# Performance work log

Hardware: AMD Instinct MI355X
Metric: run time of the kernel (lower is better)

## Reference

```python
import jax, jax.numpy as jnp
import numpy as np

N, E, G = 50000, 640000, 256
NODE_IN, EDGE_IN, EXT_IN = 32, 16, 8
H, L = 128, 3
BN_EPS = 1e-5


def _linear_init(key, fan_in, fan_out):
    kw, kb = jax.random.split(key)
    s = 1.0 / np.sqrt(fan_in)
    w = jax.random.uniform(kw, (fan_in, fan_out), minval=-s, maxval=s, dtype=jnp.float32)
    b = jax.random.uniform(kb, (fan_out,), minval=-s, maxval=s, dtype=jnp.float32)
    return w, b


def setup_inputs() -> dict:
    key = jax.random.key(0)
    ks = jax.random.split(key, 16)
    x = jax.random.normal(ks[0], (N, NODE_IN), dtype=jnp.float32)
    edge_index = jax.random.randint(ks[1], (2, E), 0, N)
    edge_attr = jax.random.normal(ks[2], (E, EDGE_IN), dtype=jnp.float32)
    batch = jnp.sort(jax.random.randint(ks[3], (N,), 0, G))
    externals = jax.random.normal(ks[4], (G, EXT_IN), dtype=jnp.float32)

    node_w, node_b = _linear_init(ks[5], NODE_IN, H)
    ee_w1, ee_b1 = _linear_init(ks[6], EDGE_IN, H)
    ee_w2, ee_b2 = _linear_init(ks[7], H, H)
    # stacked per-layer GINEConv MLP params: [L, H, H] / [L, H]
    cks = jax.random.split(ks[8], 2 * L)
    cw1, cb1, cw2, cb2 = [], [], [], []
    for l in range(L):
        w1, b1 = _linear_init(cks[2 * l], H, H)
        w2, b2 = _linear_init(cks[2 * l + 1], H, H)
        cw1.append(w1); cb1.append(b1); cw2.append(w2); cb2.append(b2)
    conv_w1 = jnp.stack(cw1); conv_b1 = jnp.stack(cb1)
    conv_w2 = jnp.stack(cw2); conv_b2 = jnp.stack(cb2)
    bn_gamma = jnp.ones((L, H), dtype=jnp.float32)
    bn_beta = jnp.zeros((L, H), dtype=jnp.float32)
    ext_w1, ext_b1 = _linear_init(ks[9], EXT_IN, H)
    ext_w2, ext_b2 = _linear_init(ks[10], H, H)
    reg_w1, reg_b1 = _linear_init(ks[11], 2 * H, H)
    reg_w2, reg_b2 = _linear_init(ks[12], H, 1)

    return dict(x=x, edge_attr=edge_attr, externals=externals,
                node_w=node_w, node_b=node_b,
                ee_w1=ee_w1, ee_b1=ee_b1, ee_w2=ee_w2, ee_b2=ee_b2,
                conv_w1=conv_w1, conv_b1=conv_b1, conv_w2=conv_w2, conv_b2=conv_b2,
                bn_gamma=bn_gamma, bn_beta=bn_beta,
                ext_w1=ext_w1, ext_b1=ext_b1, ext_w2=ext_w2, ext_b2=ext_b2,
                reg_w1=reg_w1, reg_b1=reg_b1, reg_w2=reg_w2, reg_b2=reg_b2,
                edge_index=edge_index, batch=batch, num_graphs=G)


def reference(x, edge_attr, externals,
              node_w, node_b, ee_w1, ee_b1, ee_w2, ee_b2,
              conv_w1, conv_b1, conv_w2, conv_b2, bn_gamma, bn_beta,
              ext_w1, ext_b1, ext_w2, ext_b2,
              reg_w1, reg_b1, reg_w2, reg_b2,
              edge_index, batch, num_graphs):
    n = x.shape[0]
    src, dst = edge_index[0], edge_index[1]
    h = x @ node_w + node_b                                      # [N,H]
    e = jax.nn.relu(edge_attr @ ee_w1 + ee_b1) @ ee_w2 + ee_b2   # [E,H]
    for l in range(conv_w1.shape[0]):
        # GINEConv (eps=0): aggr = sum_j relu(x_j + e_ij); out = MLP(x_i + aggr)
        msg = jax.nn.relu(h[src] + e)                            # gather + add + relu [E,H]
        aggr = jax.ops.segment_sum(msg, dst, num_segments=n)     # scatter-add [N,H]
        z = h + aggr
        z = jax.nn.relu(z @ conv_w1[l] + conv_b1[l]) @ conv_w2[l] + conv_b2[l]
        # BatchNorm1d (batch statistics)
        mean = z.mean(axis=0)
        var = z.var(axis=0)
        z = (z - mean) * jax.lax.rsqrt(var + BN_EPS) * bn_gamma[l] + bn_beta[l]
        h = jax.nn.relu(z)                                       # dropout = identity (eval)
    # global mean pool over graphs
    gsum = jax.ops.segment_sum(h, batch, num_segments=num_graphs)
    cnt = jax.ops.segment_sum(jnp.ones((n, 1), h.dtype), batch, num_segments=num_graphs)
    graph_emb = gsum / jnp.maximum(cnt, 1.0)
    ext = jax.nn.relu(externals @ ext_w1 + ext_b1) @ ext_w2 + ext_b2
    comb = jnp.concatenate([graph_emb, ext], axis=-1)            # [G,2H]
    out = jax.nn.relu(comb @ reg_w1 + reg_b1) @ reg_w2 + reg_b2  # [G,1]
    return out.squeeze(-1)
```

## Files before the change

### kernel.cpp

```cpp
#include <hip/hip_runtime.h>

typedef __bf16 bf16_t;
typedef __bf16 bf16x8 __attribute__((ext_vector_type(8)));
typedef __bf16 bf16x4 __attribute__((ext_vector_type(4)));
typedef __bf16 bf16x2 __attribute__((ext_vector_type(2)));
typedef float  f32x4  __attribute__((ext_vector_type(4)));

#define MFMA16(a, b, c) __builtin_amdgcn_mfma_f32_16x16x32_bf16((a), (b), (c), 0, 0, 0)

__global__ void prep_w_kernel(const float* __restrict__ W, bf16_t* __restrict__ Ws,
                              int Kact, int KP) {
    int idx = blockIdx.x * 256 + threadIdx.x;
    if (idx >= 128 * KP) return;
    int j    = idx & 7;
    int lane = (idx >> 3) & 63;
    int ct   = (idx >> 9) & 7;
    int kc   = idx >> 12;
    int n = ct * 16 + (lane & 15);
    int k = kc * 32 + (lane >> 4) * 8 + j;
    Ws[idx] = (bf16_t)((k < Kact) ? W[k * 128 + n] : 0.0f);
}

__global__ __launch_bounds__(256) void hist_kernel(const int* __restrict__ ei,
                                                   int* __restrict__ deg, int E) {
    int t = blockIdx.x * 256 + threadIdx.x;
    if (t < E) atomicAdd(&deg[ei[(long)E + t]], 1);
}

__global__ __launch_bounds__(256) void scanA_kernel(const int* __restrict__ deg,
                                                    int* __restrict__ partials,
                                                    int* __restrict__ bsums, int N) {
    __shared__ int s[256];
    int b = blockIdx.x, t = threadIdx.x;
    int base = b * 1024 + t * 4;
    int v0 = (base + 0 < N) ? deg[base + 0] : 0;
    int v1 = (base + 1 < N) ? deg[base + 1] : 0;
    int v2 = (base + 2 < N) ? deg[base + 2] : 0;
    int v3 = (base + 3 < N) ? deg[base + 3] : 0;
    int local = v0 + v1 + v2 + v3;
    s[t] = local;
    __syncthreads();
    for (int off = 1; off < 256; off <<= 1) {
        int v = (t >= off) ? s[t - off] : 0;
        __syncthreads();
        s[t] += v;
        __syncthreads();
    }
    int excl = s[t] - local;
    if (base + 0 < N) partials[base + 0] = excl;
    if (base + 1 < N) partials[base + 1] = excl + v0;
    if (base + 2 < N) partials[base + 2] = excl + v0 + v1;
    if (base + 3 < N) partials[base + 3] = excl + v0 + v1 + v2;
    if (t == 255) bsums[b] = s[255];
}

__global__ __launch_bounds__(256) void scanB_kernel(const int* __restrict__ bsums,
                                                    int* __restrict__ boff,
                                                    int* __restrict__ rowptr,
                                                    int NB, int N) {
    __shared__ int s[256];
    int t = threadIdx.x;
    int local = (t < NB) ? bsums[t] : 0;
    s[t] = local;
    __syncthreads();
    for (int off = 1; off < 256; off <<= 1) {
        int v = (t >= off) ? s[t - off] : 0;
        __syncthreads();
        s[t] += v;
        __syncthreads();
    }
    if (t < NB) boff[t] = s[t] - local;
    if (t == NB - 1) rowptr[N] = s[t];
}

__global__ __launch_bounds__(256) void scanC_kernel(const int* __restrict__ partials,
                                                    const int* __restrict__ boff,
                                                    int* __restrict__ rowptr,
                                                    int* __restrict__ cursor, int N) {
    int i = blockIdx.x * 256 + threadIdx.x;
    if (i >= N) return;
    int v = partials[i] + boff[i >> 10];
    rowptr[i] = v;
    cursor[i] = v;
}

__global__ __launch_bounds__(256) void scatter_kernel(const int* __restrict__ ei,
                                                      int* __restrict__ cursor,
                                                      int* __restrict__ srcp,
                                                      int* __restrict__ eorig, int E) {
    int t = blockIdx.x * 256 + threadIdx.x;
    if (t >= E) return;
    int d = ei[(long)E + t];
    int pos = atomicAdd(&cursor[d], 1);
    srcp[pos] = ei[t];
    eorig[pos] = t;
}

__global__ __launch_bounds__(256) void node_enc_kernel(
    const float* __restrict__ A, int M,
    const bf16_t* __restrict__ Ws, const float* __restrict__ bias,
    bf16_t* __restrict__ outp)
{
    constexpr int S = 136;
    __shared__ bf16_t T[128 * S];

    const int  tid  = threadIdx.x;
    const int  wv   = tid >> 6, lane = tid & 63;
    const long row0 = (long)blockIdx.x * 128;
    const int  l16  = lane & 15, quad = lane >> 4;
// ... 59 lines not shown
    const int* __restrict__ eorig, bf16_t* __restrict__ outp)
{
    constexpr int S = 136;
    __shared__ bf16_t T[64 * S];

    const int  tid  = threadIdx.x;
    const int  wv   = tid >> 6, lane = tid & 63;
    const long row0 = (long)blockIdx.x * 64;
    const int  l16  = lane & 15, quad = lane >> 4;

    {
        int  r  = wv * 16 + (lane >> 2);
        long gr = row0 + r;
        float4 v = make_float4(0.f, 0.f, 0.f, 0.f);
        if (gr < M) {
            long eo = eorig[gr];
            v = *(const float4*)(A + eo * 16 + (lane & 3) * 4);
        }
        bf16_t* d = &T[r * S + (lane & 3) * 4];
        d[0] = (bf16_t)v.x; d[1] = (bf16_t)v.y; d[2] = (bf16_t)v.z; d[3] = (bf16_t)v.w;
    }

    f32x4 acc[8];
#pragma unroll
    for (int c = 0; c < 8; c++) acc[c] = (f32x4){0.f, 0.f, 0.f, 0.f};

    {
        bf16x8 af;
#pragma unroll
        for (int j = 0; j < 8; ++j) af[j] = (bf16_t)0.f;
        if (quad < 2) af = *(const bf16x8*)&T[(wv * 16 + l16) * S + quad * 8];
#pragma unroll
        for (int c = 0; c < 8; c++) {
            bf16x8 bfr = *(const bf16x8*)&Ws1[((c * 64) + lane) * 8];
            acc[c] = MFMA16(af, bfr, acc[c]);
        }
    }

    const int mbase = wv * 16 + quad * 4;

#pragma unroll
    for (int c = 0; c < 8; c++) {
        int col = c * 16 + l16;
        float bb = b1[col];
#pragma unroll
        for (int q = 0; q < 4; q++)
            T[(mbase + q) * S + col] = (bf16_t)fmaxf(acc[c][q] + bb, 0.f);
    }

#pragma unroll
    for (int c = 0; c < 8; c++) acc[c] = (f32x4){0.f, 0.f, 0.f, 0.f};

#pragma unroll
    for (int kc = 0; kc < 4; ++kc) {
        bf16x8 af = *(const bf16x8*)&T[(wv * 16 + l16) * S + kc * 32 + quad * 8];
#pragma unroll
        for (int c = 0; c < 8; c++) {
            bf16x8 bfr = *(const bf16x8*)&Ws2[(((kc * 8 + c) * 64) + lane) * 8];
            acc[c] = MFMA16(af, bfr, acc[c]);
        }
    }

#pragma unroll
    for (int c = 0; c < 8; c++) {
        int col = c * 16 + l16;
        float bb = b2[col];
#pragma unroll
        for (int q = 0; q < 4; q++)
            T[(mbase + q) * S + col] = (bf16_t)(acc[c][q] + bb);
    }

#pragma unroll
    for (int it = 0; it < 4; ++it) {
        int idx = it * 64 + lane;
        int row = wv * 16 + (idx >> 4);
        int seg = idx & 15;
        long grow = row0 + row;
        if (grow < M)
            *(uint4*)&outp[grow * 128 + seg * 8] = *(const uint4*)&T[row * S + seg * 8];
    }
}

template <int BN>
__global__ __launch_bounds__(256) void aggr_conv_kernel(
    const bf16_t* __restrict__ xin, const float* __restrict__ scsh,
    const bf16_t* __restrict__ e,
    const int* __restrict__ rowptr, const int* __restrict__ srcp, int M,
    const bf16_t* __restrict__ Ws1, const float* __restrict__ b1,
    const bf16_t* __restrict__ Ws2, const float* __restrict__ b2,
    bf16_t* __restrict__ zout, float* __restrict__ bn_sums)
{
    constexpr int S = 136;
    __shared__ bf16_t T[64 * S];

    const int  tid  = threadIdx.x;
    const int  wv   = tid >> 6, lane = tid & 63;
    const long row0 = (long)blockIdx.x * 64;

    float sc0 = 1.f, sh0 = 0.f, sc1 = 1.f, sh1 = 0.f;
    if (BN) {
        sc0 = scsh[lane * 2];       sh0 = scsh[128 + lane * 2];
        sc1 = scsh[lane * 2 + 1];   sh1 = scsh[128 + lane * 2 + 1];
    }

    for (int r = wv * 16; r < wv * 16 + 16; ++r) {
        long n = row0 + r;
        float ax = 0.f, ay = 0.f;
        if (n < M) {
            bf16x2 xv = *(const bf16x2*)(xin + n * 128 + lane * 2);
            ax = BN ? fmaxf((float)xv[0] * sc0 + sh0, 0.f) : (float)xv[0];
            ay = BN ? fmaxf((float)xv[1] * sc1 + sh1, 0.f) : (float)xv[1];
            int beg = rowptr[n], end = rowptr[n + 1];
            for (int base = beg; base < end; base += 64) {
                int cnt = min(64, end - base);
                int sv = (base + lane < end) ? srcp[base + lane] : 0;
                int j = 0;
                for (; j + 3 < cnt; j += 4) {
                    int s0 = __shfl(sv, j), s1 = __shfl(sv, j + 1);
                    int s2 = __shfl(sv, j + 2), s3 = __shfl(sv, j + 3);
                    bf16x2 x0 = *(const bf16x2*)(xin + (long)s0 * 128 + lane * 2);
                    bf16x2 x1 = *(const bf16x2*)(xin + (long)s1 * 128 + lane * 2);
                    bf16x2 x2 = *(const bf16x2*)(xin + (long)s2 * 128 + lane * 2);
                    bf16x2 x3 = *(const bf16x2*)(xin + (long)s3 * 128 + lane * 2);
                    bf16x2 e0 = *(const bf16x2*)(e + (long)(base + j + 0) * 128 + lane * 2);
                    bf16x2 e1 = *(const bf16x2*)(e + (long)(base + j + 1) * 128 + lane * 2);
                    bf16x2 e2 = *(const bf16x2*)(e + (long)(base + j + 2) * 128 + lane * 2);
                    bf16x2 e3 = *(const bf16x2*)(e + (long)(base + j + 3) * 128 + lane * 2);
                    float hx, hy;
                    hx = BN ? fmaxf((float)x0[0] * sc0 + sh0, 0.f) : (float)x0[0];
                    hy = BN ? fmaxf((float)x0[1] * sc1 + sh1, 0.f) : (float)x0[1];
                    ax += fmaxf(hx + (float)e0[0], 0.f);
                    ay += fmaxf(hy + (float)e0[1], 0.f);
                    hx = BN ? fmaxf((float)x1[0] * sc0 + sh0, 0.f) : (float)x1[0];
                    hy = BN ? fmaxf((float)x1[1] * sc1 + sh1, 0.f) : (float)x1[1];
                    ax += fmaxf(hx + (float)e1[0], 0.f);
                    ay += fmaxf(hy + (float)e1[1], 0.f);
                    hx = BN ? fmaxf((float)x2[0] * sc0 + sh0, 0.f) : (float)x2[0];
                    hy = BN ? fmaxf((float)x2[1] * sc1 + sh1, 0.f) : (float)x2[1];
                    ax += fmaxf(hx + (float)e2[0], 0.f);
                    ay += fmaxf(hy + (float)e2[1], 0.f);
                    hx = BN ? fmaxf((float)x3[0] * sc0 + sh0, 0.f) : (float)x3[0];
                    hy = BN ? fmaxf((float)x3[1] * sc1 + sh1, 0.f) : (float)x3[1];
                    ax += fmaxf(hx + (float)e3[0], 0.f);
                    ay += fmaxf(hy + (float)e3[1], 0.f);
                }
                for (; j < cnt; ++j) {
                    int s0 = __shfl(sv, j);
                    bf16x2 x0 = *(const bf16x2*)(xin + (long)s0 * 128 + lane * 2);
                    bf16x2 e0 = *(const bf16x2*)(e + (long)(base + j) * 128 + lane * 2);
                    float hx = BN ? fmaxf((float)x0[0] * sc0 + sh0, 0.f) : (float)x0[0];
                    float hy = BN ? fmaxf((float)x0[1] * sc1 + sh1, 0.f) : (float)x0[1];
                    ax += fmaxf(hx + (float)e0[0], 0.f);
                    ay += fmaxf(hy + (float)e0[1], 0.f);
                }
            }
        }
        bf16x2 o; o[0] = (bf16_t)ax; o[1] = (bf16_t)ay;
        *(bf16x2*)&T[r * S + lane * 2] = o;
    }

    const int l16 = lane & 15, quad = lane >> 4;
    const int mbase = wv * 16 + quad * 4;

    f32x4 acc[8];
#pragma unroll
    for (int c = 0; c < 8; c++) acc[c] = (f32x4){0.f, 0.f, 0.f, 0.f};

#pragma unroll
    for (int kc = 0; kc < 4; ++kc) {
        bf16x8 af = *(const bf16x8*)&T[(wv * 16 + l16) * S + kc * 32 + quad * 8];
#pragma unroll
        for (int c = 0; c < 8; c++) {
            bf16x8 bfr = *(const bf16x8*)&Ws1[(((kc * 8 + c) * 64) + lane) * 8];
            acc[c] = MFMA16(af, bfr, acc[c]);
        }
    }

#pragma unroll
    for (int c = 0; c < 8; c++) {
        int col = c * 16 + l16;
        float bb = b1[col];
#pragma unroll
        for (int q = 0; q < 4; q++)
            T[(mbase + q) * S + col] = (bf16_t)fmaxf(acc[c][q] + bb, 0.f);
    }

#pragma unroll
    for (int c = 0; c < 8; c++) acc[c] = (f32x4){0.f, 0.f, 0.f, 0.f};

#pragma unroll
    for (int kc = 0; kc < 4; ++kc) {
        bf16x8 af = *(const bf16x8*)&T[(wv * 16 + l16) * S + kc * 32 + quad * 8];
#pragma unroll
        for (int c = 0; c < 8; c++) {
            bf16x8 bfr = *(const bf16x8*)&Ws2[(((kc * 8 + c) * 64) + lane) * 8];
            acc[c] = MFMA16(af, bfr, acc[c]);
        }
    }

    float ssum[8], ssq[8];
#pragma unroll
    for (int c = 0; c < 8; c++) {
        int col = c * 16 + l16;
        float bb = b2[col];
        float s = 0.f, s2 = 0.f;
#pragma unroll
        for (int q = 0; q < 4; q++) {
            float v = acc[c][q] + bb;
            T[(mbase + q) * S + col] = (bf16_t)v;
            if (row0 + mbase + q < M) { s += v; s2 += v * v; }
        }
        s  += __shfl_xor(s, 16);  s  += __shfl_xor(s, 32);
        s2 += __shfl_xor(s2, 16); s2 += __shfl_xor(s2, 32);
        ssum[c] = s; ssq[c] = s2;
    }

#pragma unroll
    for (int it = 0; it < 4; ++it) {
        int idx = it * 64 + lane;
        int row = wv * 16 + (idx >> 4);
        int seg = idx & 15;
        long grow = row0 + row;
        if (grow < M)
            *(uint4*)&zout[grow * 128 + seg * 8] = *(const uint4*)&T[row * S + seg * 8];
    }

    float* wred = (float*)&T[(size_t)(wv * 16) * S];
    if (quad == 0) {
#pragma unroll
        for (int c = 0; c < 8; c++) {
            int col = c * 16 + l16;
            wred[col]       = ssum[c];
            wred[128 + col] = ssq[c];
        }
    }
    __syncthreads();
    if (tid < 128) {
        float s = 0.f, s2 = 0.f;
#pragma unroll
        for (int w = 0; w < 4; ++w) {
            const float* wr = (const float*)&T[(size_t)(w * 16) * S];
            s  += wr[tid];
            s2 += wr[128 + tid];
        }
        atomicAdd(&bn_sums[tid], s);
        atomicAdd(&bn_sums[128 + tid], s2);
    }
}

__global__ void bn_fin_kernel(float* __restrict__ sums, const float* __restrict__ gamma,
                              const float* __restrict__ beta, float* __restrict__ scsh, int N)
{
    int c = threadIdx.x;
    float s  = sums[c];
    float sq = sums[128 + c];
    float mean = s / (float)N;
    float var  = sq / (float)N - mean * mean;
    float inv  = rsqrtf(var + 1e-5f);
    float sc   = gamma[c] * inv;
    scsh[c]       = sc;
    scsh[128 + c] = beta[c] - mean * sc;
    sums[c] = 0.f;
    sums[128 + c] = 0.f;
}

__global__ __launch_bounds__(128) void pool_kernel(
    const bf16_t* __restrict__ z, const float* __restrict__ scsh,
    const int* __restrict__ batch,
    float* __restrict__ gsum, float* __restrict__ cnt, int N)
{
    int c = threadIdx.x;
    float sc = scsh[c], sh = scsh[128 + c];
    int n0 = blockIdx.x * 32;
    int n1 = min(n0 + 32, N);
    float acc = 0.f;
    int cur = -1, rc = 0;
    for (int n = n0; n < n1; ++n) {
        int g = batch[n];
        if (g != cur) {
            if (cur >= 0) {
                atomicAdd(&gsum[(long)cur * 128 + c], acc);
                if (c == 0) atomicAdd(&cnt[cur], (float)rc);
            }
            cur = g; acc = 0.f; rc = 0;
        }
        acc += fmaxf((float)z[(long)n * 128 + c] * sc + sh, 0.f);
        rc++;
    }
    if (cur >= 0) {
        atomicAdd(&gsum[(long)cur * 128 + c], acc);
        if (c == 0) atomicAdd(&cnt[cur], (float)rc);
    }
}

__global__ __launch_bounds__(128) void head_kernel(
    const float* __restrict__ gsum, const float* __restrict__ cnt,
    const float* __restrict__ ext_in,
    const float* __restrict__ ew1, const float* __restrict__ eb1,
    const float* __restrict__ ew2, const float* __restrict__ eb2,
    const float* __restrict__ rw1, const float* __restrict__ rb1,
    const float* __restrict__ rw2, const float* __restrict__ rb2,
    float* __restrict__ out)
{
    int g = blockIdx.x, c = threadIdx.x;
    __shared__ float sx[8];
    __shared__ float h1[128];
    __shared__ float comb[256];
    __shared__ float red[128];

    if (c < 8) sx[c] = ext_in[g * 8 + c];
    __syncthreads();
    float a = eb1[c];
#pragma unroll
    for (int k = 0; k < 8; k++) a += sx[k] * ew1[k * 128 + c];
    h1[c] = fmaxf(a, 0.f);
    __syncthreads();
    float b = eb2[c];
    for (int k = 0; k < 128; k++) b += h1[k] * ew2[k * 128 + c];
    comb[c]       = gsum[(long)g * 128 + c] / fmaxf(cnt[g], 1.0f);
    comb[128 + c] = b;
    __syncthreads();
    float r = rb1[c];
    for (int k = 0; k < 256; k++) r += comb[k] * rw1[k * 128 + c];
    r = fmaxf(r, 0.f);
    red[c] = r * rw2[c];
    __syncthreads();
    if (c == 0) {
        float s = rb2[0];
        for (int k = 0; k < 128; k++) s += red[k];
        out[g] = s;
    }
}

extern "C" void kernel_launch(void* const* d_in, const int* in_sizes, int n_in,
                              void* d_out, int out_size, void* d_ws, size_t ws_size,
                              hipStream_t stream)
{
    const float* x         = (const float*)d_in[0];
    const float* edge_attr = (const float*)d_in[1];
    const float* externals = (const float*)d_in[2];
    const float* node_w    = (const float*)d_in[3];
    const float* node_b    = (const float*)d_in[4];
    const float* ee_w1     = (const float*)d_in[5];
    const float* ee_b1     = (const float*)d_in[6];
    const float* ee_w2     = (const float*)d_in[7];
    const float* ee_b2     = (const float*)d_in[8];
    const float* conv_w1   = (const float*)d_in[9];
    const float* conv_b1   = (const float*)d_in[10];
    const float* conv_w2   = (const float*)d_in[11];
    const float* conv_b2   = (const float*)d_in[12];
    const float* bn_gamma  = (const float*)d_in[13];
    const float* bn_beta   = (const float*)d_in[14];
    const float* ext_w1    = (const float*)d_in[15];
    const float* ext_b1    = (const float*)d_in[16];
    const float* ext_w2    = (const float*)d_in[17];
    const float* ext_b2    = (const float*)d_in[18];
    const float* reg_w1    = (const float*)d_in[19];
    const float* reg_b1    = (const float*)d_in[20];
    const float* reg_w2    = (const float*)d_in[21];
    const float* reg_b2    = (const float*)d_in[22];
    const int* edge_index  = (const int*)d_in[23];
    const int* batch       = (const int*)d_in[24];

    const int N = in_sizes[0] / 32;
    const int E = in_sizes[1] / 16;
    const int G = in_sizes[2] / 8;
    const int NB = (N + 1023) / 1024;

    char* p = (char*)d_ws;
    auto alloc = [&](size_t bytes) -> void* {
        void* r = (void*)p;
        p += (bytes + 255) & ~(size_t)255;
        return r;
    };
    bf16_t* h       = (bf16_t*)alloc((size_t)N * 128 * 2);
    bf16_t* zA      = (bf16_t*)alloc((size_t)N * 128 * 2);
    bf16_t* zB      = (bf16_t*)alloc((size_t)N * 128 * 2);
    bf16_t* ebuf    = (bf16_t*)alloc((size_t)E * 128 * 2);
    int*    deg     = (int*)alloc((size_t)N * 4);
    int*    rowptr  = (int*)alloc(((size_t)N + 1) * 4);
    int*    cursor  = (int*)alloc((size_t)N * 4);
    int*    partials= (int*)alloc((size_t)N * 4);
    int*    bsums   = (int*)alloc((size_t)NB * 4);
    int*    boff    = (int*)alloc((size_t)NB * 4);
    int*    srcp    = (int*)alloc((size_t)E * 4);
    int*    eorig   = (int*)alloc((size_t)E * 4);
    bf16_t* node_wt = (bf16_t*)alloc(128 * 32 * 2);
    bf16_t* ee_w1t  = (bf16_t*)alloc(128 * 32 * 2);
    bf16_t* ee_w2t  = (bf16_t*)alloc(128 * 128 * 2);
    bf16_t* cw1t    = (bf16_t*)alloc(3 * 128 * 128 * 2);
    bf16_t* cw2t    = (bf16_t*)alloc(3 * 128 * 128 * 2);
    float*  bn_sums = (float*)alloc(256 * 4);
    float*  scsh    = (float*)alloc(256 * 4);
    float*  gsum    = (float*)alloc((size_t)G * 128 * 4);
    float*  cnt     = (float*)alloc((size_t)G * 4);

    hipMemsetAsync(deg, 0, (size_t)N * 4, stream);
    hipMemsetAsync(bn_sums, 0, 256 * 4, stream);
    hist_kernel<<<(E + 255) / 256, 256, 0, stream>>>(edge_index, deg, E);
    scanA_kernel<<<NB, 256, 0, stream>>>(deg, partials, bsums, N);
    scanB_kernel<<<1, 256, 0, stream>>>(bsums, boff, rowptr, NB, N);
    scanC_kernel<<<(N + 255) / 256, 256, 0, stream>>>(partials, boff, rowptr, cursor, N);
    scatter_kernel<<<(E + 255) / 256, 256, 0, stream>>>(edge_index, cursor, srcp, eorig, E);

    prep_w_kernel<<<16, 256, 0, stream>>>(node_w, node_wt, 32, 32);
    prep_w_kernel<<<16, 256, 0, stream>>>(ee_w1, ee_w1t, 16, 32);
    prep_w_kernel<<<64, 256, 0, stream>>>(ee_w2, ee_w2t, 128, 128);
    for (int l = 0; l < 3; l++) {
        prep_w_kernel<<<64, 256, 0, stream>>>(conv_w1 + l * 16384, cw1t + l * 16384, 128, 128);
        prep_w_kernel<<<64, 256, 0, stream>>>(conv_w2 + l * 16384, cw2t + l * 16384, 128, 128);
    }

    node_enc_kernel<<<(N + 127) / 128, 256, 0, stream>>>(x, N, node_wt, node_b, h);

    edge_mlp_kernel<<<(E + 63) / 64, 256, 0, stream>>>(
        edge_attr, E, ee_w1t, ee_b1, ee_w2t, ee_b2, eorig, ebuf);

    const int nblk = (N + 63) / 64;
    aggr_conv_kernel<0><<<nblk, 256, 0, stream>>>(
        h, nullptr, ebuf, rowptr, srcp, N,
        cw1t + 0 * 16384, conv_b1 + 0 * 128, cw2t + 0 * 16384, conv_b2 + 0 * 128,
        zA, bn_sums);
    bn_fin_kernel<<<1, 128, 0, stream>>>(bn_sums, bn_gamma + 0 * 128, bn_beta + 0 * 128, scsh, N);
    aggr_conv_kernel<1><<<nblk, 256, 0, stream>>>(
        zA, scsh, ebuf, rowptr, srcp, N,
        cw1t + 1 * 16384, conv_b1 + 1 * 128, cw2t + 1 * 16384, conv_b2 + 1 * 128,
        zB, bn_sums);
    bn_fin_kernel<<<1, 128, 0, stream>>>(bn_sums, bn_gamma + 1 * 128, bn_beta + 1 * 128, scsh, N);
    aggr_conv_kernel<1><<<nblk, 256, 0, stream>>>(
        zB, scsh, ebuf, rowptr, srcp, N,
        cw1t + 2 * 16384, conv_b1 + 2 * 128, cw2t + 2 * 16384, conv_b2 + 2 * 128,
        zA, bn_sums);
    bn_fin_kernel<<<1, 128, 0, stream>>>(bn_sums, bn_gamma + 2 * 128, bn_beta + 2 * 128, scsh, N);

    hipMemsetAsync(gsum, 0, (size_t)G * 128 * 4, stream);
    hipMemsetAsync(cnt, 0, (size_t)G * 4, stream);
    pool_kernel<<<(N + 31) / 32, 128, 0, stream>>>(zA, scsh, batch, gsum, cnt, N);
    head_kernel<<<G, 128, 0, stream>>>(gsum, cnt, externals,
                                       ext_w1, ext_b1, ext_w2, ext_b2,
                                       reg_w1, reg_b1, reg_w2, reg_b2,
                                       (float*)d_out);
}
```

Before: 580.1 us.

## Merge weight prep launches, fold BN finalize into consumers, widen aggregation lanes

Replaces the seven weight-prep launches with one kernel. It removes the three bn_fin kernels by recomputing BN scale and shift inside each consumer from per-layer sum buffers. It restructures the aggregation loop so each half-wave handles one node with 4 channels per lane, processing two rows at a time. The hist kernel also touches edge_attr to pre-warm the cache for the later edge MLP. Together these cut launch count and change the gather access granularity, at the cost of redundant BN math per block and some masked lane work when the paired nodes have uneven degrees.

```diff
diff --git a/kernel.cpp b/kernel.cpp
--- a/kernel.cpp
+++ b/kernel.cpp
@@ -8,9 +8,24 @@
 
 #define MFMA16(a, b, c) __builtin_amdgcn_mfma_f32_16x16x32_bf16((a), (b), (c), 0, 0, 0)
 
-__global__ void prep_w_kernel(const float* __restrict__ W, bf16_t* __restrict__ Ws,
-                              int Kact, int KP) {
-    int idx = blockIdx.x * 256 + threadIdx.x;
+__global__ __launch_bounds__(256) void prep_all_kernel(
+    const float* __restrict__ nw,  const float* __restrict__ ew1,
+    const float* __restrict__ ew2, const float* __restrict__ cw1,
+    const float* __restrict__ cw2,
+    bf16_t* __restrict__ nwt,  bf16_t* __restrict__ ew1t,
+    bf16_t* __restrict__ ew2t, bf16_t* __restrict__ cw1t,
+    bf16_t* __restrict__ cw2t)
+{
+    int b = blockIdx.x;
+    const float* W; bf16_t* O; int Kact, KP, lb;
+    if (b < 16)       { W = nw;  O = nwt;  Kact = 32;  KP = 32;  lb = b; }
+    else if (b < 32)  { W = ew1; O = ew1t; Kact = 16;  KP = 32;  lb = b - 16; }
+    else if (b < 96)  { W = ew2; O = ew2t; Kact = 128; KP = 128; lb = b - 32; }
+    else if (b < 288) { int l = (b - 96) / 64;  W = cw1 + l * 16384; O = cw1t + l * 16384;
+                        Kact = 128; KP = 128; lb = (b - 96) % 64; }
+    else              { int l = (b - 288) / 64; W = cw2 + l * 16384; O = cw2t + l * 16384;
+                        Kact = 128; KP = 128; lb = (b - 288) % 64; }
+    int idx = lb * 256 + threadIdx.x;
     if (idx >= 128 * KP) return;
     int j    = idx & 7;
     int lane = (idx >> 3) & 63;
@@ -18,13 +33,19 @@
     int kc   = idx >> 12;
     int n = ct * 16 + (lane & 15);
     int k = kc * 32 + (lane >> 4) * 8 + j;
-    Ws[idx] = (bf16_t)((k < Kact) ? W[k * 128 + n] : 0.0f);
+    O[idx] = (bf16_t)((k < Kact) ? W[k * 128 + n] : 0.0f);
 }
 
 __global__ __launch_bounds__(256) void hist_kernel(const int* __restrict__ ei,
-                                                   int* __restrict__ deg, int E) {
+                                                   int* __restrict__ deg, int E,
+                                                   const float* __restrict__ ea) {
     int t = blockIdx.x * 256 + threadIdx.x;
-    if (t < E) atomicAdd(&deg[ei[(long)E + t]], 1);
+    if (t < E) {
+        atomicAdd(&deg[ei[(long)E + t]], 1);
+        float w0 = ea[(long)t * 16];
+        float w1 = ea[(long)t * 16 + 8];
+        asm volatile("" :: "v"(w0), "v"(w1));
+    }
 }
 
 __global__ __launch_bounds__(256) void scanA_kernel(const int* __restrict__ deg,
@@ -251,80 +272,104 @@
 
 template <int BN>
 __global__ __launch_bounds__(256) void aggr_conv_kernel(
-    const bf16_t* __restrict__ xin, const float* __restrict__ scsh,
+    const bf16_t* __restrict__ xin,
+    const float* __restrict__ bns_prev,
+    const float* __restrict__ gamma, const float* __restrict__ beta,
     const bf16_t* __restrict__ e,
     const int* __restrict__ rowptr, const int* __restrict__ srcp, int M,
     const bf16_t* __restrict__ Ws1, const float* __restrict__ b1,
     const bf16_t* __restrict__ Ws2, const float* __restrict__ b2,
-    bf16_t* __restrict__ zout, float* __restrict__ bn_sums)
+    bf16_t* __restrict__ zout, float* __restrict__ bn_out)
 {
     constexpr int S = 136;
     __shared__ bf16_t T[64 * S];
 
     const int  tid  = threadIdx.x;
     const int  wv   = tid >> 6, lane = tid & 63;
+    const int  half = lane >> 5, l32 = lane & 31;
+    const int  c0   = l32 * 4;
     const long row0 = (long)blockIdx.x * 64;
 
-    float sc0 = 1.f, sh0 = 0.f, sc1 = 1.f, sh1 = 0.f;
+    float sc[4], sh[4];
     if (BN) {
-        sc0 = scsh[lane * 2];       sh0 = scsh[128 + lane * 2];
-        sc1 = scsh[lane * 2 + 1];   sh1 = scsh[128 + lane * 2 + 1];
-    }
-
-    for (int r = wv * 16; r < wv * 16 + 16; ++r) {
-        long n = row0 + r;
-        float ax = 0.f, ay = 0.f;
+#pragma unroll
+        for (int u = 0; u < 4; ++u) {
+            int c = c0 + u;
+            float mean = bns_prev[c] / (float)M;
+            float var  = bns_prev[128 + c] / (float)M - mean * mean;
+            float inv  = rsqrtf(var + 1e-5f);
+            sc[u] = gamma[c] * inv;
+            sh[u] = beta[c] - mean * sc[u];
+        }
+    }
+
+#pragma unroll 1
+    for (int rp = 0; rp < 8; ++rp) {
+        int  rA = wv * 16 + rp * 2;
+        long n  = row0 + rA + half;
+        float a0 = 0.f, a1 = 0.f, a2 = 0.f, a3 = 0.f;
+        int beg = 0, cnt = 0;
         if (n < M) {
-            bf16x2 xv = *(const bf16x2*)(xin + n * 128 + lane * 2);
-            ax = BN ? fmaxf((float)xv[0] * sc0 + sh0, 0.f) : (float)xv[0];
-            ay = BN ? fmaxf((float)xv[1] * sc1 + sh1, 0.f) : (float)xv[1];
-            int beg = rowptr[n], end = rowptr[n + 1];
-            for (int base = beg; base < end; base += 64) {
-                int cnt = min(64, end - base);
-                int sv = (base + lane < end) ? srcp[base + lane] : 0;
-                int j = 0;
-                for (; j + 3 < cnt; j += 4) {
-                    int s0 = __shfl(sv, j), s1 = __shfl(sv, j + 1);
-                    int s2 = __shfl(sv, j + 2), s3 = __shfl(sv, j + 3);
-                    bf16x2 x0 = *(const bf16x2*)(xin + (long)s0 * 128 + lane * 2);
-                    bf16x2 x1 = *(const bf16x2*)(xin + (long)s1 * 128 + lane * 2);
-                    bf16x2 x2 = *(const bf16x2*)(xin + (long)s2 * 128 + lane * 2);
-                    bf16x2 x3 = *(const bf16x2*)(xin + (long)s3 * 128 + lane * 2);
-                    bf16x2 e0 = *(const bf16x2*)(e + (long)(base + j + 0) * 128 + lane * 2);
-                    bf16x2 e1 = *(const bf16x2*)(e + (long)(base + j + 1) * 128 + lane * 2);
-                    bf16x2 e2 = *(const bf16x2*)(e + (long)(base + j + 2) * 128 + lane * 2);
-                    bf16x2 e3 = *(const bf16x2*)(e + (long)(base + j + 3) * 128 + lane * 2);
-                    float hx, hy;
-                    hx = BN ? fmaxf((float)x0[0] * sc0 + sh0, 0.f) : (float)x0[0];
-                    hy = BN ? fmaxf((float)x0[1] * sc1 + sh1, 0.f) : (float)x0[1];
-                    ax += fmaxf(hx + (float)e0[0], 0.f);
-                    ay += fmaxf(hy + (float)e0[1], 0.f);
-                    hx = BN ? fmaxf((float)x1[0] * sc0 + sh0, 0.f) : (float)x1[0];
-                    hy = BN ? fmaxf((float)x1[1] * sc1 + sh1, 0.f) : (float)x1[1];
-                    ax += fmaxf(hx + (float)e1[0], 0.f);
-                    ay += fmaxf(hy + (float)e1[1], 0.f);
-                    hx = BN ? fmaxf((float)x2[0] * sc0 + sh0, 0.f) : (float)x2[0];
-                    hy = BN ? fmaxf((float)x2[1] * sc1 + sh1, 0.f) : (float)x2[1];
-                    ax += fmaxf(hx + (float)e2[0], 0.f);
-                    ay += fmaxf(hy + (float)e2[1], 0.f);
-                    hx = BN ? fmaxf((float)x3[0] * sc0 + sh0, 0.f) : (float)x3[0];
-                    hy = BN ? fmaxf((float)x3[1] * sc1 + sh1, 0.f) : (float)x3[1];
-                    ax += fmaxf(hx + (float)e3[0], 0.f);
-                    ay += fmaxf(hy + (float)e3[1], 0.f);
-                }
-                for (; j < cnt; ++j) {
-                    int s0 = __shfl(sv, j);
-                    bf16x2 x0 = *(const bf16x2*)(xin + (long)s0 * 128 + lane * 2);
-                    bf16x2 e0 = *(const bf16x2*)(e + (long)(base + j) * 128 + lane * 2);
-                    float hx = BN ? fmaxf((float)x0[0] * sc0 + sh0, 0.f) : (float)x0[0];
-                    float hy = BN ? fmaxf((float)x0[1] * sc1 + sh1, 0.f) : (float)x0[1];
-                    ax += fmaxf(hx + (float)e0[0], 0.f);
-                    ay += fmaxf(hy + (float)e0[1], 0.f);
-                }
+            beg = rowptr[n];
+            cnt = rowptr[n + 1] - beg;
+            bf16x4 xv = *(const bf16x4*)(xin + n * 128 + c0);
+            if (BN) {
+                a0 = fmaxf((float)xv[0] * sc[0] + sh[0], 0.f);
+                a1 = fmaxf((float)xv[1] * sc[1] + sh[1], 0.f);
+                a2 = fmaxf((float)xv[2] * sc[2] + sh[2], 0.f);
+                a3 = fmaxf((float)xv[3] * sc[3] + sh[3], 0.f);
+            } else {
+                a0 = (float)xv[0]; a1 = (float)xv[1];
+                a2 = (float)xv[2]; a3 = (float)xv[3];
             }
         }
-        bf16x2 o; o[0] = (bf16_t)ax; o[1] = (bf16_t)ay;
-        *(bf16x2*)&T[r * S + lane * 2] = o;
+        for (int cb = 0;; cb += 32) {
+            int rem = cnt - cb;
+            int mx  = max(rem, __shfl_xor(rem, 32));
+            if (mx <= 0) break;
+            int sv   = (cb + l32 < cnt) ? srcp[beg + cb + l32] : 0;
+            int ccnt = min(rem, 32);
+            int lim  = min(mx, 32);
+            for (int j = 0; j < lim; j += 4) {
+                int ib = (half << 5) + j;
+                int s0 = __shfl(sv, ib),     s1 = __shfl(sv, ib + 1);
+                int s2 = __shfl(sv, ib + 2), s3 = __shfl(sv, ib + 3);
+                bool v0 = j < ccnt, v1 = j + 1 < ccnt, v2 = j + 2 < ccnt, v3 = j + 3 < ccnt;
+                long eb = (long)(beg + cb + j);
+                bf16x4 x0 = *(const bf16x4*)(xin + (long)s0 * 128 + c0);
+                bf16x4 x1 = *(const bf16x4*)(xin + (long)s1 * 128 + c0);
+                bf16x4 x2 = *(const bf16x4*)(xin + (long)s2 * 128 + c0);
+                bf16x4 x3 = *(const bf16x4*)(xin + (long)s3 * 128 + c0);
+                bf16x4 e0 = *(const bf16x4*)(e + (v0 ? eb     : 0) * 128 + c0);
+                bf16x4 e1 = *(const bf16x4*)(e + (v1 ? eb + 1 : 0) * 128 + c0);
+                bf16x4 e2 = *(const bf16x4*)(e + (v2 ? eb + 2 : 0) * 128 + c0);
+                bf16x4 e3 = *(const bf16x4*)(e + (v3 ? eb + 3 : 0) * 128 + c0);
+#define ACC4(XV, EV, V)                                                        \
+                do {                                                           \
+                    float h0 = (float)XV[0], h1 = (float)XV[1];                \
+                    float h2 = (float)XV[2], h3 = (float)XV[3];                \
+                    if (BN) {                                                  \
+                        h0 = fmaxf(h0 * sc[0] + sh[0], 0.f);                   \
+                        h1 = fmaxf(h1 * sc[1] + sh[1], 0.f);                   \
+                        h2 = fmaxf(h2 * sc[2] + sh[2], 0.f);                   \
+                        h3 = fmaxf(h3 * sc[3] + sh[3], 0.f);                   \
+                    }                                                          \
+                    float t0 = fmaxf(h0 + (float)EV[0], 0.f);                  \
+                    float t1 = fmaxf(h1 + (float)EV[1], 0.f);                  \
+                    float t2 = fmaxf(h2 + (float)EV[2], 0.f);                  \
+                    float t3 = fmaxf(h3 + (float)EV[3], 0.f);                  \
+                    if (V) { a0 += t0; a1 += t1; a2 += t2; a3 += t3; }         \
+                } while (0)
+                ACC4(x0, e0, v0);
+                ACC4(x1, e1, v1);
+                ACC4(x2, e2, v2);
+                ACC4(x3, e3, v3);
+#undef ACC4
+            }
+        }
+        bf16x4 o;
+        o[0] = (bf16_t)a0; o[1] = (bf16_t)a1; o[2] = (bf16_t)a2; o[3] = (bf16_t)a3;
+        *(bf16x4*)&T[(rA + half) * S + c0] = o;
     }
 
     const int l16 = lane & 15, quad = lane >> 4;
@@ -411,34 +456,23 @@
             s  += wr[tid];
             s2 += wr[128 + tid];
         }
-        atomicAdd(&bn_sums[tid], s);
-        atomicAdd(&bn_sums[128 + tid], s2);
-    }
-}
-
-__global__ void bn_fin_kernel(float* __restrict__ sums, const float* __restrict__ gamma,
-                              const float* __restrict__ beta, float* __restrict__ scsh, int N)
-{
-    int c = threadIdx.x;
-    float s  = sums[c];
-    float sq = sums[128 + c];
-    float mean = s / (float)N;
-    float var  = sq / (float)N - mean * mean;
-    float inv  = rsqrtf(var + 1e-5f);
-    float sc   = gamma[c] * inv;
-    scsh[c]       = sc;
-    scsh[128 + c] = beta[c] - mean * sc;
-    sums[c] = 0.f;
-    sums[128 + c] = 0.f;
+        atomicAdd(&bn_out[tid], s);
+        atomicAdd(&bn_out[128 + tid], s2);
+    }
 }
 
 __global__ __launch_bounds__(128) void pool_kernel(
-    const bf16_t* __restrict__ z, const float* __restrict__ scsh,
+    const bf16_t* __restrict__ z, const float* __restrict__ bns,
+    const float* __restrict__ gamma, const float* __restrict__ beta,
     const int* __restrict__ batch,
     float* __restrict__ gsum, float* __restrict__ cnt, int N)
 {
     int c = threadIdx.x;
-    float sc = scsh[c], sh = scsh[128 + c];
+    float mean = bns[c] / (float)N;
+    float var  = bns[128 + c] / (float)N - mean * mean;
+    float inv  = rsqrtf(var + 1e-5f);
+    float sc   = gamma[c] * inv;
+    float sh   = beta[c] - mean * sc;
     int n0 = blockIdx.x * 32;
     int n1 = min(n0 + 32, N);
     float acc = 0.f;
@@ -558,26 +592,20 @@
     bf16_t* ee_w2t  = (bf16_t*)alloc(128 * 128 * 2);
     bf16_t* cw1t    = (bf16_t*)alloc(3 * 128 * 128 * 2);
     bf16_t* cw2t    = (bf16_t*)alloc(3 * 128 * 128 * 2);
-    float*  bn_sums = (float*)alloc(256 * 4);
-    float*  scsh    = (float*)alloc(256 * 4);
+    float*  bns     = (float*)alloc(3 * 256 * 4);
     float*  gsum    = (float*)alloc((size_t)G * 128 * 4);
     float*  cnt     = (float*)alloc((size_t)G * 4);
 
     hipMemsetAsync(deg, 0, (size_t)N * 4, stream);
-    hipMemsetAsync(bn_sums, 0, 256 * 4, stream);
-    hist_kernel<<<(E + 255) / 256, 256, 0, stream>>>(edge_index, deg, E);
+    hipMemsetAsync(bns, 0, 3 * 256 * 4, stream);
+    hist_kernel<<<(E + 255) / 256, 256, 0, stream>>>(edge_index, deg, E, edge_attr);
     scanA_kernel<<<NB, 256, 0, stream>>>(deg, partials, bsums, N);
     scanB_kernel<<<1, 256, 0, stream>>>(bsums, boff, rowptr, NB, N);
     scanC_kernel<<<(N + 255) / 256, 256, 0, stream>>>(partials, boff, rowptr, cursor, N);
     scatter_kernel<<<(E + 255) / 256, 256, 0, stream>>>(edge_index, cursor, srcp, eorig, E);
 
-    prep_w_kernel<<<16, 256, 0, stream>>>(node_w, node_wt, 32, 32);
-    prep_w_kernel<<<16, 256, 0, stream>>>(ee_w1, ee_w1t, 16, 32);
-    prep_w_kernel<<<64, 256, 0, stream>>>(ee_w2, ee_w2t, 128, 128);
-    for (int l = 0; l < 3; l++) {
-        prep_w_kernel<<<64, 256, 0, stream>>>(conv_w1 + l * 16384, cw1t + l * 16384, 128, 128);
-        prep_w_kernel<<<64, 256, 0, stream>>>(conv_w2 + l * 16384, cw2t + l * 16384, 128, 128);
-    }
+    prep_all_kernel<<<480, 256, 0, stream>>>(node_w, ee_w1, ee_w2, conv_w1, conv_w2,
+                                             node_wt, ee_w1t, ee_w2t, cw1t, cw2t);
 
     node_enc_kernel<<<(N + 127) / 128, 256, 0, stream>>>(x, N, node_wt, node_b, h);
 
@@ -586,24 +614,22 @@
 
     const int nblk = (N + 63) / 64;
     aggr_conv_kernel<0><<<nblk, 256, 0, stream>>>(
-        h, nullptr, ebuf, rowptr, srcp, N,
+        h, nullptr, nullptr, nullptr, ebuf, rowptr, srcp, N,
         cw1t + 0 * 16384, conv_b1 + 0 * 128, cw2t + 0 * 16384, conv_b2 + 0 * 128,
-        zA, bn_sums);
-    bn_fin_kernel<<<1, 128, 0, stream>>>(bn_sums, bn_gamma + 0 * 128, bn_beta + 0 * 128, scsh, N);
+        zA, bns + 0);
     aggr_conv_kernel<1><<<nblk, 256, 0, stream>>>(
-        zA, scsh, ebuf, rowptr, srcp, N,
+        zA, bns + 0, bn_gamma + 0, bn_beta + 0, ebuf, rowptr, srcp, N,
         cw1t + 1 * 16384, conv_b1 + 1 * 128, cw2t + 1 * 16384, conv_b2 + 1 * 128,
-        zB, bn_sums);
-    bn_fin_kernel<<<1, 128, 0, stream>>>(bn_sums, bn_gamma + 1 * 128, bn_beta + 1 * 128, scsh, N);
+        zB, bns + 256);
     aggr_conv_kernel<1><<<nblk, 256, 0, stream>>>(
-        zB, scsh, ebuf, rowptr, srcp, N,
+        zB, bns + 256, bn_gamma + 128, bn_beta + 128, ebuf, rowptr, srcp, N,
         cw1t + 2 * 16384, conv_b1 + 2 * 128, cw2t + 2 * 16384, conv_b2 + 2 * 128,
-        zA, bn_sums);
-    bn_fin_kernel<<<1, 128, 0, stream>>>(bn_sums, bn_gamma + 2 * 128, bn_beta + 2 * 128, scsh, N);
+        zA, bns + 512);
 
     hipMemsetAsync(gsum, 0, (size_t)G * 128 * 4, stream);
     hipMemsetAsync(cnt, 0, (size_t)G * 4, stream);
-    pool_kernel<<<(N + 31) / 32, 128, 0, stream>>>(zA, scsh, batch, gsum, cnt, N);
+    pool_kernel<<<(N + 31) / 32, 128, 0, stream>>>(zA, bns + 512, bn_gamma + 256, bn_beta + 256,
+                                                   batch, gsum, cnt, N);
     head_kernel<<<G, 128, 0, stream>>>(gsum, cnt, externals,
                                        ext_w1, ext_b1, ext_w2, ext_b2,
                                        reg_w1, reg_b1, reg_w2, reg_b2,
```

After: 612.0 us. 1.05x slower.

## Split aggregation across two waves per tile, fold BN finalize, merge weight prep

Applied to the files above, without the earlier changes.

The aggregation kernel moves to 512 threads so two waves share each 16-row tile for the gather, and only one wave per tile runs the MFMA MLP after a block barrier. Row pointers and source indices are prefetched one row ahead via shuffles. The BN finalize kernels are removed by computing scale and shift from per-layer sums inside the consumer kernels, and the seven weight-prep launches become one. The histogram kernel also touches edge_attr to warm the cache for the edge MLP. The trade-off is that half the waves sit idle during the MLP phase, and the extra barrier and larger blocks may reduce occupancy.

```diff
diff --git a/kernel.cpp b/kernel.cpp
--- a/kernel.cpp
+++ b/kernel.cpp
@@ -8,9 +8,24 @@
 
 #define MFMA16(a, b, c) __builtin_amdgcn_mfma_f32_16x16x32_bf16((a), (b), (c), 0, 0, 0)
 
-__global__ void prep_w_kernel(const float* __restrict__ W, bf16_t* __restrict__ Ws,
-                              int Kact, int KP) {
-    int idx = blockIdx.x * 256 + threadIdx.x;
+__global__ __launch_bounds__(256) void prep_all_kernel(
+    const float* __restrict__ nw,  const float* __restrict__ ew1,
+    const float* __restrict__ ew2, const float* __restrict__ cw1,
+    const float* __restrict__ cw2,
+    bf16_t* __restrict__ nwt,  bf16_t* __restrict__ ew1t,
+    bf16_t* __restrict__ ew2t, bf16_t* __restrict__ cw1t,
+    bf16_t* __restrict__ cw2t)
+{
+    int b = blockIdx.x;
+    const float* W; bf16_t* O; int Kact, KP, lb;
+    if (b < 16)       { W = nw;  O = nwt;  Kact = 32;  KP = 32;  lb = b; }
+    else if (b < 32)  { W = ew1; O = ew1t; Kact = 16;  KP = 32;  lb = b - 16; }
+    else if (b < 96)  { W = ew2; O = ew2t; Kact = 128; KP = 128; lb = b - 32; }
+    else if (b < 288) { int l = (b - 96) / 64;  W = cw1 + l * 16384; O = cw1t + l * 16384;
+                        Kact = 128; KP = 128; lb = (b - 96) % 64; }
+    else              { int l = (b - 288) / 64; W = cw2 + l * 16384; O = cw2t + l * 16384;
+                        Kact = 128; KP = 128; lb = (b - 288) % 64; }
+    int idx = lb * 256 + threadIdx.x;
     if (idx >= 128 * KP) return;
     int j    = idx & 7;
     int lane = (idx >> 3) & 63;
@@ -18,13 +33,19 @@
     int kc   = idx >> 12;
     int n = ct * 16 + (lane & 15);
     int k = kc * 32 + (lane >> 4) * 8 + j;
-    Ws[idx] = (bf16_t)((k < Kact) ? W[k * 128 + n] : 0.0f);
+    O[idx] = (bf16_t)((k < Kact) ? W[k * 128 + n] : 0.0f);
 }
 
 __global__ __launch_bounds__(256) void hist_kernel(const int* __restrict__ ei,
-                                                   int* __restrict__ deg, int E) {
+                                                   int* __restrict__ deg, int E,
+                                                   const float* __restrict__ ea) {
     int t = blockIdx.x * 256 + threadIdx.x;
-    if (t < E) atomicAdd(&deg[ei[(long)E + t]], 1);
+    if (t < E) {
+        atomicAdd(&deg[ei[(long)E + t]], 1);
+        float w0 = ea[(long)t * 16];
+        float w1 = ea[(long)t * 16 + 8];
+        asm volatile("" :: "v"(w0), "v"(w1));
+    }
 }
 
 __global__ __launch_bounds__(256) void scanA_kernel(const int* __restrict__ deg,
@@ -250,42 +271,76 @@
 }
 
 template <int BN>
-__global__ __launch_bounds__(256) void aggr_conv_kernel(
-    const bf16_t* __restrict__ xin, const float* __restrict__ scsh,
+__global__ __launch_bounds__(512) void aggr_conv_kernel(
+    const bf16_t* __restrict__ xin,
+    const float* __restrict__ bns_prev,
+    const float* __restrict__ gamma, const float* __restrict__ beta,
     const bf16_t* __restrict__ e,
     const int* __restrict__ rowptr, const int* __restrict__ srcp, int M,
     const bf16_t* __restrict__ Ws1, const float* __restrict__ b1,
     const bf16_t* __restrict__ Ws2, const float* __restrict__ b2,
-    bf16_t* __restrict__ zout, float* __restrict__ bn_sums)
+    bf16_t* __restrict__ zout, float* __restrict__ bn_out)
 {
     constexpr int S = 136;
     __shared__ bf16_t T[64 * S];
 
     const int  tid  = threadIdx.x;
     const int  wv   = tid >> 6, lane = tid & 63;
+    const int  tw   = wv >> 1, sub = wv & 1;
     const long row0 = (long)blockIdx.x * 64;
 
     float sc0 = 1.f, sh0 = 0.f, sc1 = 1.f, sh1 = 0.f;
     if (BN) {
-        sc0 = scsh[lane * 2];       sh0 = scsh[128 + lane * 2];
-        sc1 = scsh[lane * 2 + 1];   sh1 = scsh[128 + lane * 2 + 1];
-    }
-
-    for (int r = wv * 16; r < wv * 16 + 16; ++r) {
-        long n = row0 + r;
+        const float invM = 1.f / (float)M;
+        int c = lane * 2;
+        float m0 = bns_prev[c] * invM;
+        float v0 = bns_prev[128 + c] * invM - m0 * m0;
+        float i0 = rsqrtf(v0 + 1e-5f);
+        sc0 = gamma[c] * i0; sh0 = beta[c] - m0 * sc0;
+        float m1 = bns_prev[c + 1] * invM;
+        float v1 = bns_prev[128 + c + 1] * invM - m1 * m1;
+        float i1 = rsqrtf(v1 + 1e-5f);
+        sc1 = gamma[c + 1] * i1; sh1 = beta[c + 1] - m1 * sc1;
+    }
+
+    const long nbase = row0 + tw * 16 + sub * 8;
+    int rpv = 0;
+    {
+        long idx = nbase + lane;
+        if (idx > M) idx = M;
+        if (lane <= 8) rpv = rowptr[idx];
+    }
+
+    int sv;
+    {
+        int b0 = __shfl(rpv, 0), e0 = __shfl(rpv, 1);
+        sv = (b0 + lane < e0) ? srcp[b0 + lane] : 0;
+    }
+
+#pragma unroll 1
+    for (int r8 = 0; r8 < 8; ++r8) {
+        const int  r   = tw * 16 + sub * 8 + r8;
+        const long n   = row0 + r;
+        const int  beg = __shfl(rpv, r8);
+        const int  end = __shfl(rpv, r8 + 1);
+        int svc = sv;
+        if (r8 < 7) {
+            int nb = __shfl(rpv, r8 + 1), ne = __shfl(rpv, r8 + 2);
+            sv = (nb + lane < ne) ? srcp[nb + lane] : 0;
+        }
         float ax = 0.f, ay = 0.f;
         if (n < M) {
             bf16x2 xv = *(const bf16x2*)(xin + n * 128 + lane * 2);
             ax = BN ? fmaxf((float)xv[0] * sc0 + sh0, 0.f) : (float)xv[0];
             ay = BN ? fmaxf((float)xv[1] * sc1 + sh1, 0.f) : (float)xv[1];
-            int beg = rowptr[n], end = rowptr[n + 1];
             for (int base = beg; base < end; base += 64) {
                 int cnt = min(64, end - base);
-                int sv = (base + lane < end) ? srcp[base + lane] : 0;
+                int svv = (base == beg) ? svc
+                                        : ((base + lane < end) ? srcp[base + lane] : 0);
                 int j = 0;
                 for (; j + 3 < cnt; j += 4) {
-                    int s0 = __shfl(sv, j), s1 = __shfl(sv, j + 1);
-                    int s2 = __shfl(sv, j + 2), s3 = __shfl(sv, j + 3);
+                    int s0 = __shfl(svv, j),     s1 = __shfl(svv, j + 1);
+                    int s2 = __shfl(svv, j + 2), s3 = __shfl(svv, j + 3);
                     bf16x2 x0 = *(const bf16x2*)(xin + (long)s0 * 128 + lane * 2);
                     bf16x2 x1 = *(const bf16x2*)(xin + (long)s1 * 128 + lane * 2);
                     bf16x2 x2 = *(const bf16x2*)(xin + (long)s2 * 128 + lane * 2);
@@ -313,7 +368,7 @@
                     ay += fmaxf(hy + (float)e3[1], 0.f);
                 }
                 for (; j < cnt; ++j) {
-                    int s0 = __shfl(sv, j);
+                    int s0 = __shfl(svv, j);
                     bf16x2 x0 = *(const bf16x2*)(xin + (long)s0 * 128 + lane * 2);
                     bf16x2 e0 = *(const bf16x2*)(e + (long)(base + j) * 128 + lane * 2);
                     float hx = BN ? fmaxf((float)x0[0] * sc0 + sh0, 0.f) : (float)x0[0];
@@ -326,80 +381,83 @@
         bf16x2 o; o[0] = (bf16_t)ax; o[1] = (bf16_t)ay;
         *(bf16x2*)&T[r * S + lane * 2] = o;
     }
-
-    const int l16 = lane & 15, quad = lane >> 4;
-    const int mbase = wv * 16 + quad * 4;
-
-    f32x4 acc[8];
-#pragma unroll
-    for (int c = 0; c < 8; c++) acc[c] = (f32x4){0.f, 0.f, 0.f, 0.f};
-
-#pragma unroll
-    for (int kc = 0; kc < 4; ++kc) {
-        bf16x8 af = *(const bf16x8*)&T[(wv * 16 + l16) * S + kc * 32 + quad * 8];
-#pragma unroll
-        for (int c = 0; c < 8; c++) {
-            bf16x8 bfr = *(const bf16x8*)&Ws1[(((kc * 8 + c) * 64) + lane) * 8];
-            acc[c] = MFMA16(af, bfr, acc[c]);
-        }
-    }
-
-#pragma unroll
-    for (int c = 0; c < 8; c++) {
-        int col = c * 16 + l16;
-        float bb = b1[col];
-#pragma unroll
-        for (int q = 0; q < 4; q++)
-            T[(mbase + q) * S + col] = (bf16_t)fmaxf(acc[c][q] + bb, 0.f);
-    }
-
-#pragma unroll
-    for (int c = 0; c < 8; c++) acc[c] = (f32x4){0.f, 0.f, 0.f, 0.f};
-
-#pragma unroll
-    for (int kc = 0; kc < 4; ++kc) {
-        bf16x8 af = *(const bf16x8*)&T[(wv * 16 + l16) * S + kc * 32 + quad * 8];
-#pragma unroll
-        for (int c = 0; c < 8; c++) {
-            bf16x8 bfr = *(const bf16x8*)&Ws2[(((kc * 8 + c) * 64) + lane) * 8];
-            acc[c] = MFMA16(af, bfr, acc[c]);
-        }
-    }
-
-    float ssum[8], ssq[8];
-#pragma unroll
-    for (int c = 0; c < 8; c++) {
-        int col = c * 16 + l16;
-        float bb = b2[col];
-        float s = 0.f, s2 = 0.f;
-#pragma unroll
-        for (int q = 0; q < 4; q++) {
-            float v = acc[c][q] + bb;
-            T[(mbase + q) * S + col] = (bf16_t)v;
-            if (row0 + mbase + q < M) { s += v; s2 += v * v; }
-        }
-        s  += __shfl_xor(s, 16);  s  += __shfl_xor(s, 32);
-        s2 += __shfl_xor(s2, 16); s2 += __shfl_xor(s2, 32);
-        ssum[c] = s; ssq[c] = s2;
-    }
-
-#pragma unroll
-    for (int it = 0; it < 4; ++it) {
-        int idx = it * 64 + lane;
-        int row = wv * 16 + (idx >> 4);
-        int seg = idx & 15;
-        long grow = row0 + row;
-        if (grow < M)
-            *(uint4*)&zout[grow * 128 + seg * 8] = *(const uint4*)&T[row * S + seg * 8];
-    }
-
-    float* wred = (float*)&T[(size_t)(wv * 16) * S];
-    if (quad == 0) {
+    __syncthreads();
+
+    if (sub == 0) {
+        const int l16 = lane & 15, quad = lane >> 4;
+        const int mbase = tw * 16 + quad * 4;
+
+        f32x4 acc[8];
+#pragma unroll
+        for (int c = 0; c < 8; c++) acc[c] = (f32x4){0.f, 0.f, 0.f, 0.f};
+
+#pragma unroll
+        for (int kc = 0; kc < 4; ++kc) {
+            bf16x8 af = *(const bf16x8*)&T[(tw * 16 + l16) * S + kc * 32 + quad * 8];
+#pragma unroll
+            for (int c = 0; c < 8; c++) {
+                bf16x8 bfr = *(const bf16x8*)&Ws1[(((kc * 8 + c) * 64) + lane) * 8];
+                acc[c] = MFMA16(af, bfr, acc[c]);
+            }
+        }
+
 #pragma unroll
         for (int c = 0; c < 8; c++) {
             int col = c * 16 + l16;
-            wred[col]       = ssum[c];
-            wred[128 + col] = ssq[c];
+            float bb = b1[col];
+#pragma unroll
+            for (int q = 0; q < 4; q++)
+                T[(mbase + q) * S + col] = (bf16_t)fmaxf(acc[c][q] + bb, 0.f);
+        }
+
+#pragma unroll
+        for (int c = 0; c < 8; c++) acc[c] = (f32x4){0.f, 0.f, 0.f, 0.f};
+
+#pragma unroll
+        for (int kc = 0; kc < 4; ++kc) {
+            bf16x8 af = *(const bf16x8*)&T[(tw * 16 + l16) * S + kc * 32 + quad * 8];
+#pragma unroll
+            for (int c = 0; c < 8; c++) {
+                bf16x8 bfr = *(const bf16x8*)&Ws2[(((kc * 8 + c) * 64) + lane) * 8];
+                acc[c] = MFMA16(af, bfr, acc[c]);
+            }
+        }
+
+        float ssum[8], ssq[8];
+#pragma unroll
+        for (int c = 0; c < 8; c++) {
+            int col = c * 16 + l16;
+            float bb = b2[col];
+            float s = 0.f, s2 = 0.f;
+#pragma unroll
+            for (int q = 0; q < 4; q++) {
+                float v = acc[c][q] + bb;
+                T[(mbase + q) * S + col] = (bf16_t)v;
+                if (row0 + mbase + q < M) { s += v; s2 += v * v; }
+            }
+            s  += __shfl_xor(s, 16);  s  += __shfl_xor(s, 32);
+            s2 += __shfl_xor(s2, 16); s2 += __shfl_xor(s2, 32);
+            ssum[c] = s; ssq[c] = s2;
+        }
+
+#pragma unroll
+        for (int it = 0; it < 4; ++it) {
+            int idx = it * 64 + lane;
+            int row = tw * 16 + (idx >> 4);
+            int seg = idx & 15;
+            long grow = row0 + row;
+            if (grow < M)
+                *(uint4*)&zout[grow * 128 + seg * 8] = *(const uint4*)&T[row * S + seg * 8];
+        }
+
+        float* wred = (float*)&T[(size_t)(tw * 16) * S];
+        if (quad == 0) {
+#pragma unroll
+            for (int c = 0; c < 8; c++) {
+                int col = c * 16 + l16;
+                wred[col]       = ssum[c];
+                wred[128 + col] = ssq[c];
+            }
         }
     }
     __syncthreads();
@@ -411,34 +469,23 @@
             s  += wr[tid];
             s2 += wr[128 + tid];
         }
-        atomicAdd(&bn_sums[tid], s);
-        atomicAdd(&bn_sums[128 + tid], s2);
-    }
-}
-
-__global__ void bn_fin_kernel(float* __restrict__ sums, const float* __restrict__ gamma,
-                              const float* __restrict__ beta, float* __restrict__ scsh, int N)
-{
-    int c = threadIdx.x;
-    float s  = sums[c];
-    float sq = sums[128 + c];
-    float mean = s / (float)N;
-    float var  = sq / (float)N - mean * mean;
-    float inv  = rsqrtf(var + 1e-5f);
-    float sc   = gamma[c] * inv;
-    scsh[c]       = sc;
-    scsh[128 + c] = beta[c] - mean * sc;
-    sums[c] = 0.f;
-    sums[128 + c] = 0.f;
+        atomicAdd(&bn_out[tid], s);
+        atomicAdd(&bn_out[128 + tid], s2);
+    }
 }
 
 __global__ __launch_bounds__(128) void pool_kernel(
-    const bf16_t* __restrict__ z, const float* __restrict__ scsh,
+    const bf16_t* __restrict__ z, const float* __restrict__ bns,
+    const float* __restrict__ gamma, const float* __restrict__ beta,
     const int* __restrict__ batch,
     float* __restrict__ gsum, float* __restrict__ cnt, int N)
 {
     int c = threadIdx.x;
-    float sc = scsh[c], sh = scsh[128 + c];
+    float mean = bns[c] / (float)N;
+    float var  = bns[128 + c] / (float)N - mean * mean;
+    float inv  = rsqrtf(var + 1e-5f);
+    float sc   = gamma[c] * inv;
+    float sh   = beta[c] - mean * sc;
     int n0 = blockIdx.x * 32;
     int n1 = min(n0 + 32, N);
     float acc = 0.f;
@@ -558,26 +605,20 @@
     bf16_t* ee_w2t  = (bf16_t*)alloc(128 * 128 * 2);
     bf16_t* cw1t    = (bf16_t*)alloc(3 * 128 * 128 * 2);
     bf16_t* cw2t    = (bf16_t*)alloc(3 * 128 * 128 * 2);
-    float*  bn_sums = (float*)alloc(256 * 4);
-    float*  scsh    = (float*)alloc(256 * 4);
+    float*  bns     = (float*)alloc(3 * 256 * 4);
     float*  gsum    = (float*)alloc((size_t)G * 128 * 4);
     float*  cnt     = (float*)alloc((size_t)G * 4);
 
     hipMemsetAsync(deg, 0, (size_t)N * 4, stream);
-    hipMemsetAsync(bn_sums, 0, 256 * 4, stream);
-    hist_kernel<<<(E + 255) / 256, 256, 0, stream>>>(edge_index, deg, E);
+    hipMemsetAsync(bns, 0, 3 * 256 * 4, stream);
+    hist_kernel<<<(E + 255) / 256, 256, 0, stream>>>(edge_index, deg, E, edge_attr);
     scanA_kernel<<<NB, 256, 0, stream>>>(deg, partials, bsums, N);
     scanB_kernel<<<1, 256, 0, stream>>>(bsums, boff, rowptr, NB, N);
     scanC_kernel<<<(N + 255) / 256, 256, 0, stream>>>(partials, boff, rowptr, cursor, N);
     scatter_kernel<<<(E + 255) / 256, 256, 0, stream>>>(edge_index, cursor, srcp, eorig, E);
 
-    prep_w_kernel<<<16, 256, 0, stream>>>(node_w, node_wt, 32, 32);
-    prep_w_kernel<<<16, 256, 0, stream>>>(ee_w1, ee_w1t, 16, 32);
-    prep_w_kernel<<<64, 256, 0, stream>>>(ee_w2, ee_w2t, 128, 128);
-    for (int l = 0; l < 3; l++) {
-        prep_w_kernel<<<64, 256, 0, stream>>>(conv_w1 + l * 16384, cw1t + l * 16384, 128, 128);
-        prep_w_kernel<<<64, 256, 0, stream>>>(conv_w2 + l * 16384, cw2t + l * 16384, 128, 128);
-    }
+    prep_all_kernel<<<480, 256, 0, stream>>>(node_w, ee_w1, ee_w2, conv_w1, conv_w2,
+                                             node_wt, ee_w1t, ee_w2t, cw1t, cw2t);
 
     node_enc_kernel<<<(N + 127) / 128, 256, 0, stream>>>(x, N, node_wt, node_b, h);
 
@@ -585,25 +626,23 @@
         edge_attr, E, ee_w1t, ee_b1, ee_w2t, ee_b2, eorig, ebuf);
 
     const int nblk = (N + 63) / 64;
-    aggr_conv_kernel<0><<<nblk, 256, 0, stream>>>(
-        h, nullptr, ebuf, rowptr, srcp, N,
+    aggr_conv_kernel<0><<<nblk, 512, 0, stream>>>(
+        h, nullptr, nullptr, nullptr, ebuf, rowptr, srcp, N,
         cw1t + 0 * 16384, conv_b1 + 0 * 128, cw2t + 0 * 16384, conv_b2 + 0 * 128,
-        zA, bn_sums);
-    bn_fin_kernel<<<1, 128, 0, stream>>>(bn_sums, bn_gamma + 0 * 128, bn_beta + 0 * 128, scsh, N);
-    aggr_conv_kernel<1><<<nblk, 256, 0, stream>>>(
-        zA, scsh, ebuf, rowptr, srcp, N,
+        zA, bns + 0);
+    aggr_conv_kernel<1><<<nblk, 512, 0, stream>>>(
+        zA, bns + 0, bn_gamma + 0, bn_beta + 0, ebuf, rowptr, srcp, N,
         cw1t + 1 * 16384, conv_b1 + 1 * 128, cw2t + 1 * 16384, conv_b2 + 1 * 128,
-        zB, bn_sums);
-    bn_fin_kernel<<<1, 128, 0, stream>>>(bn_sums, bn_gamma + 1 * 128, bn_beta + 1 * 128, scsh, N);
-    aggr_conv_kernel<1><<<nblk, 256, 0, stream>>>(
-        zB, scsh, ebuf, rowptr, srcp, N,
+        zB, bns + 256);
+    aggr_conv_kernel<1><<<nblk, 512, 0, stream>>>(
+        zB, bns + 256, bn_gamma + 128, bn_beta + 128, ebuf, rowptr, srcp, N,
         cw1t + 2 * 16384, conv_b1 + 2 * 128, cw2t + 2 * 16384, conv_b2 + 2 * 128,
-        zA, bn_sums);
-    bn_fin_kernel<<<1, 128, 0, stream>>>(bn_sums, bn_gamma + 2 * 128, bn_beta + 2 * 128, scsh, N);
+        zA, bns + 512);
 
     hipMemsetAsync(gsum, 0, (size_t)G * 128 * 4, stream);
     hipMemsetAsync(cnt, 0, (size_t)G * 4, stream);
-    pool_kernel<<<(N + 31) / 32, 128, 0, stream>>>(zA, scsh, batch, gsum, cnt, N);
+    pool_kernel<<<(N + 31) / 32, 128, 0, stream>>>(zA, bns + 512, bn_gamma + 256, bn_beta + 256,
+                                                   batch, gsum, cnt, N);
     head_kernel<<<G, 128, 0, stream>>>(gsum, cnt, externals,
                                        ext_w1, ext_b1, ext_w2, ext_b2,
                                        reg_w1, reg_b1, reg_w2, reg_b2,
```

After: 578.6 us. No clear change (-0.3%).
